# Kernel optimization log

Measured on AMD Instinct MI355X. Metric: run time of the kernel, lower is better.

The kernel has to match this reference:

```python
import jax, jax.numpy as jnp
import numpy as np

EMBED_DIM = 128
NUM_SYMBOLS = 100000  # pad_idx = NUM_SYMBOLS, table has NUM_SYMBOLS+1 rows
BATCH = 1024
MAX_NBR = 200
LN_EPS = 1e-5


def setup_inputs() -> dict:
    key = jax.random.key(0)
    ks = jax.random.split(key, 8)
    entity = jax.random.randint(ks[0], (BATCH, 2), 0, NUM_SYMBOLS)
    conn_left = jax.random.randint(ks[1], (BATCH, MAX_NBR, 2), 0, NUM_SYMBOLS)
    conn_right = jax.random.randint(ks[2], (BATCH, MAX_NBR, 2), 0, NUM_SYMBOLS)
    emb = jax.random.normal(ks[3], (NUM_SYMBOLS + 1, EMBED_DIM), jnp.float32) * 0.02
    emb = emb.at[NUM_SYMBOLS].set(0.0)  # padding row
    W_bil = jax.random.normal(ks[4], (EMBED_DIM, EMBED_DIM), jnp.float32) * 0.05
    W_tail = jax.random.normal(ks[5], (EMBED_DIM, EMBED_DIM), jnp.float32) * 0.05
    W_head = jax.random.normal(ks[6], (EMBED_DIM, EMBED_DIM), jnp.float32) * 0.05
    gamma = jnp.ones((EMBED_DIM,), jnp.float32)
    beta = jnp.zeros((EMBED_DIM,), jnp.float32)
    return {"entity": entity, "conn_left": conn_left, "conn_right": conn_right,
            "emb": emb, "W_bil": W_bil, "W_tail": W_tail, "W_head": W_head,
            "gamma": gamma, "beta": beta}


def reference(entity, conn_left, conn_right, emb, W_bil, W_tail, W_head, gamma, beta):
    pad_idx = emb.shape[0] - 1
    ent = emb[entity]                      # [b, 2, d]
    head_left, head_right = ent[:, 0], ent[:, 1]
    weak_rel = head_right - head_left      # task_emb is None -> difference

    def intra(conn):
        rel_ids, ent_ids = conn[..., 0], conn[..., 1]
        rel = emb[rel_ids]                 # [b, m, d]
        tail = emb[ent_ids]                # [b, m, d]
        mask = rel_ids == pad_idx          # [b, m]
        # Bilinear score: weak_rel^T W rel  -> [b, m]
        score = jnp.einsum('bd,de,bme->bm', weak_rel, W_bil, rel)
        score = jnp.where(mask, -jnp.inf, score)
        att = jax.nn.softmax(score, axis=1)
        return jnp.einsum('bm,bmd->bd', att, tail)

    def branch(agg, head):
        h = jax.nn.relu(agg @ W_tail.T + head @ W_head.T)
        x = h + head                       # residual (dropout is identity in eval)
        mu = jnp.mean(x, axis=-1, keepdims=True)
        var = jnp.var(x, axis=-1, keepdims=True)
        return (x - mu) * jax.lax.rsqrt(var + LN_EPS) * gamma + beta

    left = branch(intra(conn_left), head_left)
    right = branch(intra(conn_right), head_right)
    return left, right
```

## Files before the change

kernel.cpp:

```cpp
#include <hip/hip_runtime.h>

#define BATCH 1024
#define DIM 128
#define MNBR 200
#define PAD_IDX 100000
#define LN_EPS 1e-5f

#define NROWS (PAD_IDX + 1)
#define EMB_ELEMS ((size_t)NROWS * DIM)
#define WS_NEED_BYTES EMB_ELEMS
#define QCLAMP 0.125f
#define QSCALE (QCLAMP / 127.f)
#define QINV   (127.f / QCLAMP)

__device__ __forceinline__ float waveReduceSum(float v) {
    #pragma unroll
    for (int off = 32; off > 0; off >>= 1) v += __shfl_xor(v, off, 64);
    return v;
}

__device__ __forceinline__ float4 unpack_s8(int w) {
    return make_float4((float)((w << 24) >> 24), (float)((w << 16) >> 24),
                       (float)((w <<  8) >> 24), (float)( w        >> 24));
}

__global__ __launch_bounds__(256) void k0_quant(
    const float* __restrict__ emb, signed char* __restrict__ q)
{
    const size_t base = (size_t)blockIdx.x * 4096 + (size_t)threadIdx.x * 4;
    #pragma unroll
    for (int k = 0; k < 4; ++k) {
        const size_t idx = base + (size_t)k * 1024;
        if (idx < EMB_ELEMS) {
            const float4 a = *reinterpret_cast<const float4*>(emb + idx);
            const int q0 = max(-127, min(127, __float2int_rn(a.x * QINV)));
            const int q1 = max(-127, min(127, __float2int_rn(a.y * QINV)));
            const int q2 = max(-127, min(127, __float2int_rn(a.z * QINV)));
            const int q3 = max(-127, min(127, __float2int_rn(a.w * QINV)));
            const unsigned o = (unsigned)(q0 & 0xff) | ((unsigned)(q1 & 0xff) << 8)
                             | ((unsigned)(q2 & 0xff) << 16) | ((unsigned)(q3 & 0xff) << 24);
            *reinterpret_cast<unsigned*>(q + idx) = o;
        }
    }
}

__global__ __launch_bounds__(256, 4) void ee2_kernel_q8(
    const int* __restrict__ entity,
    const int* __restrict__ conn_left, const int* __restrict__ conn_right,
    const float* __restrict__ emb, const signed char* __restrict__ emb8,
    const float* __restrict__ W_bil, const float* __restrict__ W_tail,
    const float* __restrict__ W_head,
    const float* __restrict__ gamma, const float* __restrict__ beta,
    float* __restrict__ out)
{
    __shared__ int2  cidx[MNBR];
    __shared__ float wr[DIM], hs[DIM];
    __shared__ float vp[2][DIM];
    __shared__ float vsh[DIM];
    __shared__ float accp[4][DIM];
    __shared__ float lsw[4];
    __shared__ float aggs[DIM];
    __shared__ float yp[2][DIM], hp[2][DIM];
    __shared__ float redS[4], redQ[4];

    const int blk  = blockIdx.x;
    const int b    = blk >> 1;
    const int side = blk & 1;
    const int tid  = threadIdx.x;

    const int* conn = side ? conn_right : conn_left;
    if (tid < 100) {
        const int4 c = *reinterpret_cast<const int4*>(conn + (size_t)b * MNBR * 2 + tid * 4);
        cidx[tid * 2 + 0] = make_int2(c.x, c.y);
        cidx[tid * 2 + 1] = make_int2(c.z, c.w);
    } else if (tid >= 128) {
        const int t  = tid - 128;
        const int e0 = entity[b * 2 + 0], e1 = entity[b * 2 + 1];
        const float h0 = emb[(size_t)e0 * DIM + t];
        const float h1 = emb[(size_t)e1 * DIM + t];
        wr[t] = h1 - h0;
        hs[t] = side ? h1 : h0;
    }
    __syncthreads();

    {
        const int e = tid & 127, part = tid >> 7;
        float acc = 0.f;
        const int d0 = part * 64;
        #pragma unroll 8
        for (int d = d0; d < d0 + 64; ++d)
            acc += wr[d] * W_bil[(size_t)d * DIM + e];
        vp[part][e] = acc;
    }
    __syncthreads();
    if (tid < DIM) vsh[tid] = vp[0][tid] + vp[1][tid];
    __syncthreads();

    {
        const int q   = tid & 7;
        const int sub = tid >> 3;
        const int w   = tid >> 6;

        const float4 vA = *reinterpret_cast<const float4*>(&vsh[(q << 4) + 0]);
        const float4 vB = *reinterpret_cast<const float4*>(&vsh[(q << 4) + 4]);
        const float4 vC = *reinterpret_cast<const float4*>(&vsh[(q << 4) + 8]);
        const float4 vD = *reinterpret_cast<const float4*>(&vsh[(q << 4) + 12]);
        const signed char* ebq = emb8 + (q << 4);

        float acc[16];
        #pragma unroll
        for (int k = 0; k < 16; ++k) acc[k] = 0.f;
        float ls = 0.f;

        #pragma unroll
        for (int i = 0; i < 7; ++i) {
            const int  m   = sub + (i << 5);
            const bool act = (m < MNBR);
            const int  rid = act ? cidx[m].x : PAD_IDX;
            const int  eid = act ? cidx[m].y : PAD_IDX;
            const int4 rq = *reinterpret_cast<const int4*>(ebq + ((size_t)rid << 7));
            const int4 tq = *reinterpret_cast<const int4*>(ebq + ((size_t)eid << 7));

            const float4 u0 = unpack_s8(rq.x), u1 = unpack_s8(rq.y);
            const float4 u2 = unpack_s8(rq.z), u3 = unpack_s8(rq.w);
            float d0 = u0.x * vA.x + u0.y * vA.y + u0.z * vA.z + u0.w * vA.w;
            float d1 = u1.x * vB.x + u1.y * vB.y + u1.z * vB.z + u1.w * vB.w;
            float d2 = u2.x * vC.x + u2.y * vC.y + u2.z * vC.z + u2.w * vC.w;
            float d3 = u3.x * vD.x + u3.y * vD.y + u3.z * vD.z + u3.w * vD.w;
            float dot = (d0 + d1) + (d2 + d3);
            dot += __shfl_xor(dot, 1, 64);
            dot += __shfl_xor(dot, 2, 64);
            dot += __shfl_xor(dot, 4, 64);

            const float p  = (rid == PAD_IDX) ? 0.f : __expf(dot * QSCALE);
            const float ps = p * QSCALE;
            ls += p;

            const float4 t0 = unpack_s8(tq.x), t1 = unpack_s8(tq.y);
            const float4 t2 = unpack_s8(tq.z), t3 = unpack_s8(tq.w);
            acc[ 0] = fmaf(ps, t0.x, acc[ 0]); acc[ 1] = fmaf(ps, t0.y, acc[ 1]);
            acc[ 2] = fmaf(ps, t0.z, acc[ 2]); acc[ 3] = fmaf(ps, t0.w, acc[ 3]);
            acc[ 4] = fmaf(ps, t1.x, acc[ 4]); acc[ 5] = fmaf(ps, t1.y, acc[ 5]);
            acc[ 6] = fmaf(ps, t1.z, acc[ 6]); acc[ 7] = fmaf(ps, t1.w, acc[ 7]);
            acc[ 8] = fmaf(ps, t2.x, acc[ 8]); acc[ 9] = fmaf(ps, t2.y, acc[ 9]);
            acc[10] = fmaf(ps, t2.z, acc[10]); acc[11] = fmaf(ps, t2.w, acc[11]);
            acc[12] = fmaf(ps, t3.x, acc[12]); acc[13] = fmaf(ps, t3.y, acc[13]);
            acc[14] = fmaf(ps, t3.z, acc[14]); acc[15] = fmaf(ps, t3.w, acc[15]);
        }

        #pragma unroll
        for (int off = 8; off <= 32; off <<= 1) {
            #pragma unroll
            for (int k = 0; k < 16; ++k) acc[k] += __shfl_xor(acc[k], off, 64);
            ls += __shfl_xor(ls, off, 64);
        }
        if ((tid & 63) < 8) {
            #pragma unroll
            for (int k = 0; k < 4; ++k)
                *reinterpret_cast<float4*>(&accp[w][(q << 4) + (k << 2)]) =
                    make_float4(acc[k * 4], acc[k * 4 + 1], acc[k * 4 + 2], acc[k * 4 + 3]);
        }
        if ((tid & 63) == 0) lsw[w] = ls;
    }
    __syncthreads();

    if (tid < DIM) {
        const float lt = (lsw[0] + lsw[1]) + (lsw[2] + lsw[3]);
        aggs[tid] = ((accp[0][tid] + accp[1][tid]) + (accp[2][tid] + accp[3][tid])) / lt;
    }
    __syncthreads();

    {
        const int e = tid & 127, part = tid >> 7;
        const int d0 = part * 64;
        const float* wt = W_tail + (size_t)e * DIM + d0;
        const float* wh = W_head + (size_t)e * DIM + d0;
        float ya = 0.f, ha = 0.f;
        #pragma unroll 8
        for (int d = 0; d < 64; ++d) {
            ya = fmaf(aggs[d0 + d], wt[d], ya);
            ha = fmaf(hs[d0 + d],   wh[d], ha);
        }
        yp[part][e] = ya; hp[part][e] = ha;
    }
    __syncthreads();

    {
        float xv = 0.f;
        if (tid < DIM)
            xv = fmaxf((yp[0][tid] + yp[1][tid]) + (hp[0][tid] + hp[1][tid]), 0.f) + hs[tid];
        const float sum = waveReduceSum(xv);
        const float sq  = waveReduceSum(xv * xv);
        const int w = tid >> 6;
        if ((tid & 63) == 0) { redS[w] = sum; redQ[w] = sq; }
        __syncthreads();
        if (tid < DIM) {
            const float tS = redS[0] + redS[1];
            const float tQ = redQ[0] + redQ[1];
            const float mean = tS * (1.f / DIM);
            const float var  = tQ * (1.f / DIM) - mean * mean;
            out[(size_t)side * BATCH * DIM + (size_t)b * DIM + tid] =
                (xv - mean) * rsqrtf(var + LN_EPS) * gamma[tid] + beta[tid];
        }
    }
}

__global__ __launch_bounds__(512, 8) void ee_kernel_f32(
    const int* __restrict__ entity,
    const int* __restrict__ conn_left, const int* __restrict__ conn_right,
    const float* __restrict__ emb,
    const float* __restrict__ W_bil, const float* __restrict__ W_tail,
    const float* __restrict__ W_head,
    const float* __restrict__ gamma, const float* __restrict__ beta,
    float* __restrict__ out)
{
    __shared__ float wr[DIM], h0s[DIM], h1s[DIM];
    __shared__ float vp[4][DIM];
    __shared__ float v[DIM];
    __shared__ float hh[2][DIM];
    __shared__ int2  cidx[2][MNBR];
    __shared__ float accp[16][DIM];
    __shared__ float lp[16];
    __shared__ float agg[2][DIM];
    __shared__ float x[2][DIM];
    __shared__ float redS[8], redQ[8];

    const int b   = blockIdx.x;
    const int tid = threadIdx.x;
    const int g   = tid >> 5;
    const int l   = tid & 31;

    if (tid < DIM) {
        const int e0 = entity[b * 2 + 0], e1 = entity[b * 2 + 1];
        const float hl = emb[(size_t)e0 * DIM + tid];
        const float hr = emb[(size_t)e1 * DIM + tid];
        wr[tid] = hr - hl; h0s[tid] = hl; h1s[tid] = hr;
    } else if (tid < 128 + 100) {
        const int t = tid - 128;
        const int4 c = *reinterpret_cast<const int4*>(conn_left + (size_t)b * MNBR * 2 + t * 4);
        cidx[0][t * 2 + 0] = make_int2(c.x, c.y);
        cidx[0][t * 2 + 1] = make_int2(c.z, c.w);
    } else if (tid < 128 + 200) {
        const int t = tid - 228;
        const int4 c = *reinterpret_cast<const int4*>(conn_right + (size_t)b * MNBR * 2 + t * 4);
        cidx[1][t * 2 + 0] = make_int2(c.x, c.y);
        cidx[1][t * 2 + 1] = make_int2(c.z, c.w);
    }
    __syncthreads();
    {
        const int e = tid & 127, part = tid >> 7;
        float acc = 0.f;
        const int d0 = part * 32;
        #pragma unroll 8
        for (int d = d0; d < d0 + 32; ++d)
            acc += wr[d] * W_bil[(size_t)d * DIM + e];
        vp[part][e] = acc;
    }
    __syncthreads();
    if (tid < DIM) v[tid] = (vp[0][tid] + vp[1][tid]) + (vp[2][tid] + vp[3][tid]);
    {
        const float4 a4 = *reinterpret_cast<const float4*>(&h0s[l * 4]);
        const float4 b4 = *reinterpret_cast<const float4*>(&h1s[l * 4]);
        #pragma unroll
        for (int i = 0; i < 8; ++i) {
            const int e = g + i * 16;
            const float4 wh = *reinterpret_cast<const float4*>(W_head + (size_t)e * DIM + l * 4);
            float d0 = a4.x * wh.x + a4.y * wh.y + a4.z * wh.z + a4.w * wh.w;
            float d1 = b4.x * wh.x + b4.y * wh.y + b4.z * wh.z + b4.w * wh.w;
            #pragma unroll
            for (int off = 16; off > 0; off >>= 1) {
                d0 += __shfl_xor(d0, off, 64);
                d1 += __shfl_xor(d1, off, 64);
            }
            if (l == 0) { hh[0][e] = d0; hh[1][e] = d1; }
        }
    }
    __syncthreads();
    {
        const int side  = g >> 3;
        const int m0    = (g & 7) * 25;
        const float4 v4 = *reinterpret_cast<const float4*>(&v[l * 4]);
        const int2* ci  = cidx[side];
        float a0 = 0.f, a1 = 0.f, a2 = 0.f, a3 = 0.f, ls = 0.f;
        #pragma unroll 5
        for (int m = m0; m < m0 + 25; ++m) {
            const int rid = ci[m].x, eid = ci[m].y;
            const float4 r = *reinterpret_cast<const float4*>(emb + (size_t)rid * DIM + l * 4);
            const float4 t = *reinterpret_cast<const float4*>(emb + (size_t)eid * DIM + l * 4);
            float dot = v4.x * r.x + v4.y * r.y + v4.z * r.z + v4.w * r.w;
            #pragma unroll
            for (int off = 16; off > 0; off >>= 1) dot += __shfl_xor(dot, off, 64);
            const float p = (rid == PAD_IDX) ? 0.f : __expf(dot);
            ls += p;
            a0 = fmaf(p, t.x, a0); a1 = fmaf(p, t.y, a1);
            a2 = fmaf(p, t.z, a2); a3 = fmaf(p, t.w, a3);
        }
        *reinterpret_cast<float4*>(&accp[g][l * 4]) = make_float4(a0, a1, a2, a3);
        if (l == 0) lp[g] = ls;
    }
    __syncthreads();
    if (tid < 256) {
        const int s = tid >> 7, d = tid & 127;
        const int gb = s * 8;
        float lt = 0.f, a = 0.f;
        #pragma unroll
        for (int i = 0; i < 8; ++i) { lt += lp[gb + i]; a += accp[gb + i][d]; }
        agg[s][d] = a / lt;
    }
    __syncthreads();
    {
        const float4 a0v = *reinterpret_cast<const float4*>(&agg[0][l * 4]);
        const float4 a1v = *reinterpret_cast<const float4*>(&agg[1][l * 4]);
        #pragma unroll
        for (int i = 0; i < 8; ++i) {
            const int e = g + i * 16;
            const float4 wt = *reinterpret_cast<const float4*>(W_tail + (size_t)e * DIM + l * 4);
            float d0 = a0v.x * wt.x + a0v.y * wt.y + a0v.z * wt.z + a0v.w * wt.w;
            float d1 = a1v.x * wt.x + a1v.y * wt.y + a1v.z * wt.z + a1v.w * wt.w;
            #pragma unroll
            for (int off = 16; off > 0; off >>= 1) {
                d0 += __shfl_xor(d0, off, 64);
                d1 += __shfl_xor(d1, off, 64);
            }
            if (l == 0) {
                x[0][e] = fmaxf(d0 + hh[0][e], 0.f) + h0s[e];
                x[1][e] = fmaxf(d1 + hh[1][e], 0.f) + h1s[e];
            }
        }
    }
    __syncthreads();
    {
        const int s = tid >> 8;
        const int d = tid & 255;
        const int w = tid >> 6;
        float xv = 0.f;
        if (d < DIM) xv = x[s][d];
        float sum = waveReduceSum(xv);
        float sq  = waveReduceSum(xv * xv);
        if ((tid & 63) == 0) { redS[w] = sum; redQ[w] = sq; }
        __syncthreads();
        if (d < DIM) {
            const float tS = redS[s * 4] + redS[s * 4 + 1];
            const float tQ = redQ[s * 4] + redQ[s * 4 + 1];
            const float mean = tS * (1.f / DIM);
            const float var  = tQ * (1.f / DIM) - mean * mean;
            out[(size_t)s * BATCH * DIM + (size_t)b * DIM + d] =
                (xv - mean) * rsqrtf(var + LN_EPS) * gamma[d] + beta[d];
        }
    }
}

extern "C" void kernel_launch(void* const* d_in, const int* in_sizes, int n_in,
                              void* d_out, int out_size, void* d_ws, size_t ws_size,
                              hipStream_t stream) {
    const int*   entity = (const int*)d_in[0];
    const int*   cl     = (const int*)d_in[1];
    const int*   cr     = (const int*)d_in[2];
    const float* emb    = (const float*)d_in[3];
    const float* W_bil  = (const float*)d_in[4];
    const float* W_tail = (const float*)d_in[5];
    const float* W_head = (const float*)d_in[6];
    const float* gamma  = (const float*)d_in[7];
    const float* beta   = (const float*)d_in[8];
    float* out = (float*)d_out;

    if (ws_size >= WS_NEED_BYTES) {
        signed char* emb8 = (signed char*)d_ws;
        const int nblk = (int)((EMB_ELEMS + 4095) / 4096);
        k0_quant<<<nblk, 256, 0, stream>>>(emb, emb8);
        ee2_kernel_q8<<<BATCH * 2, 256, 0, stream>>>(
            entity, cl, cr, emb, emb8, W_bil, W_tail, W_head, gamma, beta, out);
    } else {
        ee_kernel_f32<<<BATCH, 512, 0, stream>>>(
            entity, cl, cr, emb, W_bil, W_tail, W_head, gamma, beta, out);
    }
}
```

Baseline: 153.5 us.

## Stage int8 neighbor rows into LDS via async global_load_lds before bilinear GEMV

Issues asynchronous global-to-LDS loads (global_load_lds) for all 400 int8 relation/tail rows right after the index fetch, so these gathers overlap with the W_bil matrix-vector product. The attention loop then reads from shared memory, using 16 lanes per row with 8 elements each instead of 8 lanes with 16. This hides gather latency but adds about 53KB of LDS per block, which can reduce occupancy. It also relies on the barrier to order the async LDS writes before they are read.

```diff
diff --git a/kernel.cpp b/kernel.cpp
--- a/kernel.cpp
+++ b/kernel.cpp
@@ -13,15 +13,16 @@
 #define QSCALE (QCLAMP / 127.f)
 #define QINV   (127.f / QCLAMP)
 
+#define NSTG 13
+
 __device__ __forceinline__ float waveReduceSum(float v) {
     #pragma unroll
     for (int off = 32; off > 0; off >>= 1) v += __shfl_xor(v, off, 64);
     return v;
 }
 
-__device__ __forceinline__ float4 unpack_s8(int w) {
-    return make_float4((float)((w << 24) >> 24), (float)((w << 16) >> 24),
-                       (float)((w <<  8) >> 24), (float)( w        >> 24));
+__device__ __forceinline__ float s8f(int w, int k) {
+    return (float)((w << ((3 - k) * 8)) >> 24);
 }
 
 __global__ __launch_bounds__(256) void k0_quant(
@@ -44,7 +45,7 @@
     }
 }
 
-__global__ __launch_bounds__(256, 4) void ee2_kernel_q8(
+__global__ __launch_bounds__(256, 4) void ee4_kernel_q8(
     const int* __restrict__ entity,
     const int* __restrict__ conn_left, const int* __restrict__ conn_right,
     const float* __restrict__ emb, const signed char* __restrict__ emb8,
@@ -53,10 +54,10 @@
     const float* __restrict__ gamma, const float* __restrict__ beta,
     float* __restrict__ out)
 {
+    __shared__ int4  stage[416][8];
     __shared__ int2  cidx[MNBR];
     __shared__ float wr[DIM], hs[DIM];
     __shared__ float vp[2][DIM];
-    __shared__ float vsh[DIM];
     __shared__ float accp[4][DIM];
     __shared__ float lsw[4];
     __shared__ float aggs[DIM];
@@ -67,6 +68,8 @@
     const int b    = blk >> 1;
     const int side = blk & 1;
     const int tid  = threadIdx.x;
+    const int w    = tid >> 6;
+    const int lane = tid & 63;
 
     const int* conn = side ? conn_right : conn_left;
     if (tid < 100) {
@@ -84,6 +87,23 @@
     __syncthreads();
 
     {
+        const int srow = lane >> 3;
+        const int soff = (lane & 7) << 4;
+        #pragma unroll
+        for (int k = 0; k < NSTG; ++k) {
+            const int r = k * 32 + w * 8 + srow;
+            int id = PAD_IDX;
+            if (r < MNBR)          id = cidx[r].x;
+            else if (r < 2 * MNBR) id = cidx[r - MNBR].y;
+            const signed char* gp = emb8 + ((size_t)id << 7) + soff;
+            __builtin_amdgcn_global_load_lds(
+                (const __attribute__((address_space(1))) unsigned int*)gp,
+                (__attribute__((address_space(3))) unsigned int*)&stage[k * 32 + w * 8][0],
+                16, 0, 0);
+        }
+    }
+
+    {
         const int e = tid & 127, part = tid >> 7;
         float acc = 0.f;
         const int d0 = part * 64;
@@ -93,74 +113,61 @@
         vp[part][e] = acc;
     }
     __syncthreads();
-    if (tid < DIM) vsh[tid] = vp[0][tid] + vp[1][tid];
-    __syncthreads();
-
-    {
-        const int q   = tid & 7;
-        const int sub = tid >> 3;
-        const int w   = tid >> 6;
-
-        const float4 vA = *reinterpret_cast<const float4*>(&vsh[(q << 4) + 0]);
-        const float4 vB = *reinterpret_cast<const float4*>(&vsh[(q << 4) + 4]);
-        const float4 vC = *reinterpret_cast<const float4*>(&vsh[(q << 4) + 8]);
-        const float4 vD = *reinterpret_cast<const float4*>(&vsh[(q << 4) + 12]);
-        const signed char* ebq = emb8 + (q << 4);
-
-        float acc[16];
-        #pragma unroll
-        for (int k = 0; k < 16; ++k) acc[k] = 0.f;
+
+    {
+        const int s = lane >> 4;
+        const int q = lane & 15;
+        float vreg[8];
+        #pragma unroll
+        for (int k = 0; k < 8; ++k) vreg[k] = vp[0][q * 8 + k] + vp[1][q * 8 + k];
+
+        float acc[8];
+        #pragma unroll
+        for (int k = 0; k < 8; ++k) acc[k] = 0.f;
         float ls = 0.f;
 
         #pragma unroll
-        for (int i = 0; i < 7; ++i) {
-            const int  m   = sub + (i << 5);
-            const bool act = (m < MNBR);
-            const int  rid = act ? cidx[m].x : PAD_IDX;
-            const int  eid = act ? cidx[m].y : PAD_IDX;
-            const int4 rq = *reinterpret_cast<const int4*>(ebq + ((size_t)rid << 7));
-            const int4 tq = *reinterpret_cast<const int4*>(ebq + ((size_t)eid << 7));
-
-            const float4 u0 = unpack_s8(rq.x), u1 = unpack_s8(rq.y);
-            const float4 u2 = unpack_s8(rq.z), u3 = unpack_s8(rq.w);
-            float d0 = u0.x * vA.x + u0.y * vA.y + u0.z * vA.z + u0.w * vA.w;
-            float d1 = u1.x * vB.x + u1.y * vB.y + u1.z * vB.z + u1.w * vB.w;
-            float d2 = u2.x * vC.x + u2.y * vC.y + u2.z * vC.z + u2.w * vC.w;
-            float d3 = u3.x * vD.x + u3.y * vD.y + u3.z * vD.z + u3.w * vD.w;
-            float dot = (d0 + d1) + (d2 + d3);
+        for (int i = 0; i < 13; ++i) {
+            const int m   = i * 16 + w * 4 + s;
+            const int rid = (m < MNBR) ? cidx[m].x : PAD_IDX;
+            const signed char* rrow = (const signed char*)&stage[m][0];
+            const signed char* trow = (const signed char*)&stage[MNBR + m][0];
+            const int2 rq = *reinterpret_cast<const int2*>(rrow + q * 8);
+            const int2 tq = *reinterpret_cast<const int2*>(trow + q * 8);
+
+            float dot = 0.f;
+            #pragma unroll
+            for (int k = 0; k < 4; ++k) dot = fmaf(s8f(rq.x, k), vreg[k], dot);
+            #pragma unroll
+            for (int k = 0; k < 4; ++k) dot = fmaf(s8f(rq.y, k), vreg[4 + k], dot);
             dot += __shfl_xor(dot, 1, 64);
             dot += __shfl_xor(dot, 2, 64);
             dot += __shfl_xor(dot, 4, 64);
+            dot += __shfl_xor(dot, 8, 64);
 
             const float p  = (rid == PAD_IDX) ? 0.f : __expf(dot * QSCALE);
             const float ps = p * QSCALE;
             ls += p;
 
-            const float4 t0 = unpack_s8(tq.x), t1 = unpack_s8(tq.y);
-            const float4 t2 = unpack_s8(tq.z), t3 = unpack_s8(tq.w);
-            acc[ 0] = fmaf(ps, t0.x, acc[ 0]); acc[ 1] = fmaf(ps, t0.y, acc[ 1]);
-            acc[ 2] = fmaf(ps, t0.z, acc[ 2]); acc[ 3] = fmaf(ps, t0.w, acc[ 3]);
-            acc[ 4] = fmaf(ps, t1.x, acc[ 4]); acc[ 5] = fmaf(ps, t1.y, acc[ 5]);
-            acc[ 6] = fmaf(ps, t1.z, acc[ 6]); acc[ 7] = fmaf(ps, t1.w, acc[ 7]);
-            acc[ 8] = fmaf(ps, t2.x, acc[ 8]); acc[ 9] = fmaf(ps, t2.y, acc[ 9]);
-            acc[10] = fmaf(ps, t2.z, acc[10]); acc[11] = fmaf(ps, t2.w, acc[11]);
-            acc[12] = fmaf(ps, t3.x, acc[12]); acc[13] = fmaf(ps, t3.y, acc[13]);
-            acc[14] = fmaf(ps, t3.z, acc[14]); acc[15] = fmaf(ps, t3.w, acc[15]);
-        }
-
-        #pragma unroll
-        for (int off = 8; off <= 32; off <<= 1) {
-            #pragma unroll
-            for (int k = 0; k < 16; ++k) acc[k] += __shfl_xor(acc[k], off, 64);
+            #pragma unroll
+            for (int k = 0; k < 4; ++k) acc[k]     = fmaf(ps, s8f(tq.x, k), acc[k]);
+            #pragma unroll
+            for (int k = 0; k < 4; ++k) acc[4 + k] = fmaf(ps, s8f(tq.y, k), acc[4 + k]);
+        }
+
+        #pragma unroll
+        for (int off = 16; off <= 32; off <<= 1) {
+            #pragma unroll
+            for (int k = 0; k < 8; ++k) acc[k] += __shfl_xor(acc[k], off, 64);
             ls += __shfl_xor(ls, off, 64);
         }
-        if ((tid & 63) < 8) {
-            #pragma unroll
-            for (int k = 0; k < 4; ++k)
-                *reinterpret_cast<float4*>(&accp[w][(q << 4) + (k << 2)]) =
-                    make_float4(acc[k * 4], acc[k * 4 + 1], acc[k * 4 + 2], acc[k * 4 + 3]);
-        }
-        if ((tid & 63) == 0) lsw[w] = ls;
+        if (lane < 16) {
+            *reinterpret_cast<float4*>(&accp[w][q * 8 + 0]) =
+                make_float4(acc[0], acc[1], acc[2], acc[3]);
+            *reinterpret_cast<float4*>(&accp[w][q * 8 + 4]) =
+                make_float4(acc[4], acc[5], acc[6], acc[7]);
+        }
+        if (lane == 0) lsw[w] = ls;
     }
     __syncthreads();
 
@@ -191,8 +198,8 @@
             xv = fmaxf((yp[0][tid] + yp[1][tid]) + (hp[0][tid] + hp[1][tid]), 0.f) + hs[tid];
         const float sum = waveReduceSum(xv);
         const float sq  = waveReduceSum(xv * xv);
-        const int w = tid >> 6;
-        if ((tid & 63) == 0) { redS[w] = sum; redQ[w] = sq; }
+        const int ww = tid >> 6;
+        if ((tid & 63) == 0) { redS[ww] = sum; redQ[ww] = sq; }
         __syncthreads();
         if (tid < DIM) {
             const float tS = redS[0] + redS[1];
@@ -368,7 +375,7 @@
         signed char* emb8 = (signed char*)d_ws;
         const int nblk = (int)((EMB_ELEMS + 4095) / 4096);
         k0_quant<<<nblk, 256, 0, stream>>>(emb, emb8);
-        ee2_kernel_q8<<<BATCH * 2, 256, 0, stream>>>(
+        ee4_kernel_q8<<<BATCH * 2, 256, 0, stream>>>(
             entity, cl, cr, emb, emb8, W_bil, W_tail, W_head, gamma, beta, out);
     } else {
         ee_kernel_f32<<<BATCH, 512, 0, stream>>>(
```

Result: slower. 165.6 us (+7.9%).
